# Optimization experiments

Measured on AMD Instinct MI355X. Metric: run time of the kernel, lower is better.

## Reference

```python
import jax, jax.numpy as jnp
import numpy as np

B, S, D = 2, 2048, 2048
H, DN, DR, DV, R = 16, 128, 64, 128, 512
EPS = 1e-6


def rmsnorm(x, g, eps=EPS):
    var = jnp.mean(x * x, axis=-1, keepdims=True)
    return x * jax.lax.rsqrt(var + eps) * g


def apply_rope(x, freqs):
    # x: [B,S,H,DR], freqs: [S, DR//2] angles. Complex-pair (interleaved) rotation.
    b, s, h, d = x.shape
    xp = x.reshape(b, s, h, d // 2, 2)
    xr, xi = xp[..., 0], xp[..., 1]
    cos = jnp.cos(freqs)[None, :, None, :]
    sin = jnp.sin(freqs)[None, :, None, :]
    outr = xr * cos - xi * sin
    outi = xr * sin + xi * cos
    return jnp.stack([outr, outi], axis=-1).reshape(b, s, h, d)


def setup_inputs() -> dict:
    key = jax.random.key(0)
    ks = jax.random.split(key, 8)
    x = jax.random.normal(ks[0], (B, S, D), dtype=jnp.float32)
    # RoPE angles: pos * inv_freq, standard theta=10000
    inv_freq = 1.0 / (10000.0 ** (np.arange(0, DR, 2, dtype=np.float32) / DR))
    freqs = jnp.asarray(np.arange(S, dtype=np.float32)[:, None] * inv_freq[None, :])
    sc = lambda fan_in: 1.0 / np.sqrt(fan_in)
    # weights stored [in, out] so forward is x @ W
    w_kv = jax.random.normal(ks[1], (D, R), dtype=jnp.float32) * sc(D)
    g_kv = jnp.ones((R,), dtype=jnp.float32)
    w_k = jax.random.normal(ks[2], (R, H * (DN + DR)), dtype=jnp.float32) * sc(R)
    w_v = jax.random.normal(ks[3], (R, H * DV), dtype=jnp.float32) * sc(R)
    w_qn = jax.random.normal(ks[4], (D, H * DN), dtype=jnp.float32) * sc(D)
    w_qr = jax.random.normal(ks[5], (D, H * DR), dtype=jnp.float32) * sc(D)
    w_o = jax.random.normal(ks[6], (H * DV, D), dtype=jnp.float32) * sc(H * DV)
    return {"x": x, "freqs": freqs, "w_kv": w_kv, "g_kv": g_kv, "w_k": w_k,
            "w_v": w_v, "w_qn": w_qn, "w_qr": w_qr, "w_o": w_o}


def reference(x, freqs, w_kv, g_kv, w_k, w_v, w_qn, w_qr, w_o):
    b, s, _ = x.shape
    # latent KV compression + RMSNorm
    kv = rmsnorm(x @ w_kv, g_kv)                       # [B,S,R]
    k_full = (kv @ w_k).reshape(b, s, H, DN + DR)      # [B,S,H,192]
    k_nope, k_rope = k_full[..., :DN], k_full[..., DN:]
    v = (kv @ w_v).reshape(b, s, H, DV)                # [B,S,H,DV]
    q_nope = (x @ w_qn).reshape(b, s, H, DN)
    q_rope = (x @ w_qr).reshape(b, s, H, DR)
    q_rope = apply_rope(q_rope, freqs)
    k_rope = apply_rope(k_rope, freqs)
    q = jnp.concatenate([q_nope, q_rope], axis=-1)     # [B,S,H,192]
    k = jnp.concatenate([k_nope, k_rope], axis=-1)
    scale = 1.0 / np.sqrt(DN + DR)
    scores = jnp.einsum('bshd,bthd->bhst', q, k) * scale  # [B,H,S,S]
    causal = jnp.tril(jnp.ones((s, s), dtype=bool))
    scores = jnp.where(causal[None, None], scores, jnp.float32(-1e30))
    attn = jax.nn.softmax(scores, axis=-1)
    out = jnp.einsum('bhst,bthd->bshd', attn, v).reshape(b, s, H * DV)
    return out @ w_o                                   # [B,S,D]
```

## Files before the change

### kernel.cpp

```cpp
#include <hip/hip_runtime.h>

typedef __bf16 bf16_t;
typedef bf16_t bf16x8 __attribute__((ext_vector_type(8)));
typedef bf16_t bf16x4v __attribute__((ext_vector_type(4)));
typedef float f32x4 __attribute__((ext_vector_type(4)));

#define GLDS16(g, l) __builtin_amdgcn_global_load_lds( \
    (const __attribute__((address_space(1))) void*)(g), \
    (__attribute__((address_space(3))) void*)(l), 16, 0, 0)

#define BB 2
#define SEQ 2048
#define DMODEL 2048
#define RDIM 512
#define NH 16
#define DNOPE 128
#define DROPE 64
#define DVDIM 128
#define MROWS 4096
#define DQK 192
#define KSTRIDE 3072


__global__ __launch_bounds__(256) void cast_x_kernel(const float* __restrict__ x,
                                                     bf16_t* __restrict__ xb) {
    int idx = blockIdx.x * 256 + threadIdx.x;
    float4 v = ((const float4*)x)[idx];
    bf16x4v o;
    o[0] = (bf16_t)v.x; o[1] = (bf16_t)v.y; o[2] = (bf16_t)v.z; o[3] = (bf16_t)v.w;
    ((bf16x4v*)xb)[idx] = o;
}

__global__ __launch_bounds__(256) void wtrans3_kernel(const float* __restrict__ W0,
                                                      const float* __restrict__ W1,
                                                      const float* __restrict__ W2,
                                                      int N0, int N1, int N2,
                                                      int b1, int b2,
                                                      bf16_t* __restrict__ WT, int K) {
    __shared__ float t[32][33];
    int n0 = blockIdx.x * 32, k0 = blockIdx.y * 32;
    const float* W; int Nsrc, cb;
    if (n0 < b1)      { W = W0; Nsrc = N0; cb = 0; }
    else if (n0 < b2) { W = W1; Nsrc = N1; cb = b1; }
    else              { W = W2; Nsrc = N2; cb = b2; }
    int col = n0 - cb;
    int tx = threadIdx.x & 31, ty = threadIdx.x >> 5;
    #pragma unroll
    for (int i = 0; i < 4; ++i)
        t[ty + i*8][tx] = W[(size_t)(k0 + ty + i*8) * Nsrc + col + tx];
    __syncthreads();
    #pragma unroll
    for (int i = 0; i < 4; ++i)
        WT[(size_t)(n0 + ty + i*8) * K + k0 + tx] = (bf16_t)t[tx][ty + i*8];
}

__global__ __launch_bounds__(256) void rope_table_kernel(const float* __restrict__ freqs,
                                                         float* __restrict__ costab,
                                                         float* __restrict__ sintab) {
    int idx = blockIdx.x * 256 + threadIdx.x;
    float f = freqs[idx];
    costab[idx] = cosf(f);
    sintab[idx] = sinf(f);
}

__global__ __launch_bounds__(256) void rmsnorm_kernel(const float* __restrict__ kvf,
                                                      const float* __restrict__ gkv,
                                                      bf16_t* __restrict__ kvb) {
    int m = blockIdx.x;
    int tid = threadIdx.x;
    const float* rowp = kvf + (size_t)m * RDIM;
    float2 v = *(const float2*)(rowp + tid * 2);
    float ss = v.x * v.x + v.y * v.y;
    #pragma unroll
    for (int d = 1; d < 64; d <<= 1) ss += __shfl_xor(ss, d, 64);
    __shared__ float red[4];
    if ((tid & 63) == 0) red[tid >> 6] = ss;
    __syncthreads();
    float tot = red[0] + red[1] + red[2] + red[3];
    float scale = rsqrtf(tot * (1.0f / RDIM) + 1e-6f);
    bf16_t* orow = kvb + (size_t)m * RDIM;
    orow[tid*2]     = (bf16_t)(v.x * scale * gkv[tid*2]);
    orow[tid*2 + 1] = (bf16_t)(v.y * scale * gkv[tid*2 + 1]);
}


template<typename OutT, int EPI>
__global__ __launch_bounds__(256, 3) void gemm_bt(const bf16_t* __restrict__ A,
                                                  const bf16_t* __restrict__ Bt,
                                                  OutT* __restrict__ C,
                                                  int M, int N, int K,
                                                  const float* __restrict__ costab,
                                                  const float* __restrict__ sintab,
                                                  bf16_t* __restrict__ C2) {
    __shared__ __align__(16) char ldsA[128 * 128];
    __shared__ __align__(16) char ldsB[128 * 128];
    int tid = threadIdx.x;
    int lane = tid & 63, wave = tid >> 6;
    int n0 = blockIdx.x * 128, m0 = blockIdx.y * 128;
    int wr = wave >> 1, wc = wave & 1;
    int g = lane >> 4, c = lane & 15;
    f32x4 acc[4][4] = {};

    int srow = tid >> 3;
    int sch = tid & 7;

    int nkt = K >> 6;
    for (int kt = 0; kt < nkt; ++kt) {
        int k0 = kt << 6;
        #pragma unroll
        for (int j = 0; j < 4; ++j) {
            int row = j * 32 + srow;
            int csrc = sch ^ (row & 7);
            const char* gA = (const char*)(A + (size_t)(m0 + row) * K + k0) + csrc * 16;
            const char* gB = (const char*)(Bt + (size_t)(n0 + row) * K + k0) + csrc * 16;
            char* lA = ldsA + j * 4096 + wave * 1024;
            char* lB = ldsB + j * 4096 + wave * 1024;
            GLDS16(gA, lA);
            GLDS16(gB, lB);
        }
        __syncthreads();
        #pragma unroll
        for (int kk = 0; kk < 2; ++kk) {
            int kb = kk * 64 + g * 16;
            bf16x8 aF[4], bF[4];
            #pragma unroll
            for (int m = 0; m < 4; ++m) {
                int row = wr * 64 + m * 16 + c;
                aF[m] = *(const bf16x8*)(ldsA + row * 128 + (kb ^ ((row & 7) << 4)));
            }
            #pragma unroll
            for (int n = 0; n < 4; ++n) {
                int row = wc * 64 + n * 16 + c;
                bF[n] = *(const bf16x8*)(ldsB + row * 128 + (kb ^ ((row & 7) << 4)));
            }
            #pragma unroll
            for (int m = 0; m < 4; ++m)
                #pragma unroll
                for (int n = 0; n < 4; ++n)
                    acc[m][n] = __builtin_amdgcn_mfma_f32_16x16x32_bf16(aF[m], bF[n], acc[m][n], 0, 0, 0);
        }
        __syncthreads();
    }
    #pragma unroll
    for (int m = 0; m < 4; ++m) {
        int grow0 = m0 + wr * 64 + m * 16 + g * 4;
        #pragma unroll
        for (int n = 0; n < 4; ++n) {
            int gcol = n0 + wc * 64 + n * 16 + c;
            if (EPI == 1) {
                if (gcol < 3072) {
                    bool rope = (gcol % 192) >= 128;
                    if (rope) {
                        int j = ((gcol % 192) - 128) >> 1;
                        bool even = (c & 1) == 0;
                        #pragma unroll
                        for (int i = 0; i < 4; ++i) {
                            float v = acc[m][n][i];
                            float pv = __shfl_xor(v, 1, 64);
                            int s = (grow0 + i) & (SEQ - 1);
                            float cs = costab[s * 32 + j], sn = sintab[s * 32 + j];
                            float o = even ? (v * cs - pv * sn) : (pv * sn + v * cs);
                            C[(size_t)(grow0 + i) * KSTRIDE + gcol] = (OutT)o;
                        }
                    } else {
                        #pragma unroll
                        for (int i = 0; i < 4; ++i)
                            C[(size_t)(grow0 + i) * KSTRIDE + gcol] = (OutT)acc[m][n][i];
                    }
                } else {
                    int vcol = gcol - 3072;
                    int hh = vcol >> 7, dv = vcol & 127;
                    int bb = grow0 >> 11, s = grow0 & (SEQ - 1);
                    bf16x4v o;
                    #pragma unroll
                    for (int i = 0; i < 4; ++i) o[i] = (bf16_t)acc[m][n][i];
                    *(bf16x4v*)(C2 + ((size_t)(bb * NH + hh) * 128 + dv) * SEQ + s) = o;
                }
            } else if (EPI == 3) {
                if (gcol < 512) {
                    #pragma unroll
                    for (int i = 0; i < 4; ++i)
                        C[(size_t)(grow0 + i) * 512 + gcol] = (OutT)acc[m][n][i];
                } else {
                    int qcol = gcol - 512;
                    if (qcol >= 2048) {
                        int j = ((qcol - 2048) & 63) >> 1;
                        bool even = (c & 1) == 0;
                        #pragma unroll
                        for (int i = 0; i < 4; ++i) {
                            float v = acc[m][n][i];
                            float pv = __shfl_xor(v, 1, 64);
                            int s = (grow0 + i) & (SEQ - 1);
                            float cs = costab[s * 32 + j], sn = sintab[s * 32 + j];
                            float o = even ? (v * cs - pv * sn) : (pv * sn + v * cs);
                            C2[(size_t)(grow0 + i) * 3072 + qcol] = (bf16_t)o;
                        }
                    } else {
                        #pragma unroll
                        for (int i = 0; i < 4; ++i)
                            C2[(size_t)(grow0 + i) * 3072 + qcol] = (bf16_t)acc[m][n][i];
                    }
                }
            } else {
                #pragma unroll
                for (int i = 0; i < 4; ++i)
                    C[(size_t)(grow0 + i) * N + gcol] = (OutT)acc[m][n][i];
            }
        }
    }
}


__global__ __launch_bounds__(512, 2) void attn_kernel(const bf16_t* __restrict__ Qf,
                                                      const bf16_t* __restrict__ KV,
                                                      const bf16_t* __restrict__ VT,
                                                      bf16_t* __restrict__ O) {
    __shared__ __align__(16) char ldsK[3 * 64 * 384];
    __shared__ __align__(16) char ldsV[3 * 128 * 128];
    __shared__ __align__(16) char ldsP[8 * 16 * 176];
    int tid = threadIdx.x, lane = tid & 63, wave = tid >> 6;
    int g = lane >> 4, c = lane & 15;

    int bid = blockIdx.x;
    int xcd = bid & 7, r = bid >> 3;
    int bh = xcd * 4 + (r & 3);
    int p = r >> 2;
    int b = bh >> 4, h = bh & 15;

    const bf16_t* Kb = KV + (size_t)b * SEQ * KSTRIDE + h * DQK;
    const bf16_t* Vb = VT + (size_t)bh * 128 * SEQ;
    char* ldsPw = ldsP + wave * (16 * 176);

    size_t soff[3];
    #pragma unroll
    for (int i2 = 0; i2 < 3; ++i2) {
        int id = i2 * 512 + tid;
        int row = id / 24, ch = id - row * 24;
        soff[i2] = (size_t)row * (KSTRIDE * 2) + (ch ^ (row & 7)) * 16;
    }
    size_t voff[2];
    #pragma unroll
    for (int i2 = 0; i2 < 2; ++i2) {
        int id = i2 * 512 + tid;
        int row = id >> 3, ch = id & 7;
        voff[i2] = (size_t)row * (SEQ * 2) + (ch ^ (row & 7)) * 16;
    }
    const float sc = 0.0721687836f * 1.44269504f;

    bf16x8 vones;
    #pragma unroll
    for (int j = 0; j < 8; ++j) vones[j] = (bf16_t)1.0f;

    auto stage = [&](int t, int buf) {
        const char* Kt = (const char*)Kb + (size_t)t * (64 * KSTRIDE * 2);
        #pragma unroll
        for (int i2 = 0; i2 < 3; ++i2)
            GLDS16(Kt + soff[i2], ldsK + buf * 24576 + i2 * 8192 + wave * 1024);
        const char* Vt = (const char*)Vb + (size_t)t * 128;
        #pragma unroll
        for (int i2 = 0; i2 < 2; ++i2)
            GLDS16(Vt + voff[i2], ldsV + buf * 16384 + i2 * 8192 + wave * 1024);
    };

    #pragma unroll 1
    for (int pass = 0; pass < 2; ++pass) {
        int qt = pass ? p : (15 - p);
        int q0 = qt * 128;
        int nt = 2 * qt + 2;
        int tdiag = 2 * qt + (wave >> 2);

        bf16x8 qf[6];
        {
            int qrow = q0 + wave * 16 + c;
            const bf16_t* qn = Qf + (size_t)(b * SEQ + qrow) * 3072 + h * DNOPE + g * 8;
            #pragma unroll
            for (int kk = 0; kk < 4; ++kk) qf[kk] = *(const bf16x8*)(qn + kk * 32);
            const bf16_t* qr = Qf + (size_t)(b * SEQ + qrow) * 3072 + 2048 + h * DROPE + g * 8;
            qf[4] = *(const bf16x8*)(qr);
            qf[5] = *(const bf16x8*)(qr + 32);
            #pragma unroll
            for (int kk = 0; kk < 6; ++kk)
                #pragma unroll
                for (int j = 0; j < 8; ++j)
                    qf[kk][j] = (bf16_t)((float)qf[kk][j] * sc);
        }
        float m_run[4];
        f32x4 accO[9] = {};
        #pragma unroll
        for (int i = 0; i < 4; ++i) m_run[i] = -3.0e38f;

        stage(0, 0);
        stage(1, 1);

        #pragma unroll 1
        for (int t = 0; t < nt; ++t) {
            int cur = t - (t / 3) * 3;
            if (t + 1 < nt) asm volatile("s_waitcnt vmcnt(5)" ::: "memory");
            else            asm volatile("s_waitcnt vmcnt(0)" ::: "memory");
            __builtin_amdgcn_s_barrier();
            __builtin_amdgcn_sched_barrier(0);
            asm volatile("" ::: "memory");
            if (t + 2 < nt) stage(t + 2, (t + 2) % 3);

            if (t <= tdiag) {
                bool diag = (t == tdiag);
                const char* ldsKc = ldsK + cur * 24576;
                const char* ldsVc = ldsV + cur * 16384;

                f32x4 accS[4] = {};
                __builtin_amdgcn_s_setprio(1);
                #pragma unroll
                for (int kk = 0; kk < 6; ++kk) {
                    int kb = kk * 64 + g * 16;
                    #pragma unroll
                    for (int n = 0; n < 4; ++n) {
                        int row = n * 16 + c;
                        bf16x8 kf = *(const bf16x8*)(ldsKc + row * 384 + (kb ^ ((row & 7) << 4)));
                        accS[n] = __builtin_amdgcn_mfma_f32_16x16x32_bf16(qf[kk], kf, accS[n], 0, 0, 0);
                    }
                }
                __builtin_amdgcn_s_setprio(0);

                if (diag) {
                    #pragma unroll
                    for (int n = 0; n < 4; ++n)
                        #pragma unroll
                        for (int i = 0; i < 4; ++i)
                            if (n * 16 + c > (wave & 3) * 16 + g * 4 + i) accS[n][i] = -1e30f;
                }
                float mloc[4];
                #pragma unroll
                for (int i = 0; i < 4; ++i)
                    mloc[i] = fmaxf(fmaxf(accS[0][i], accS[1][i]), fmaxf(accS[2][i], accS[3][i]));
                bool cheap = __all((mloc[0] <= m_run[0] + 8.f) & (mloc[1] <= m_run[1] + 8.f) &
                                   (mloc[2] <= m_run[2] + 8.f) & (mloc[3] <= m_run[3] + 8.f));
                if (cheap) {
                    #pragma unroll
                    for (int i = 0; i < 4; ++i)
                        #pragma unroll
                        for (int n = 0; n < 4; ++n)
                            accS[n][i] = exp2f(accS[n][i] - m_run[i]);
                } else {
                    #pragma unroll
                    for (int i = 0; i < 4; ++i) {
                        float m2 = mloc[i];
                        #pragma unroll
                        for (int d = 1; d < 16; d <<= 1) m2 = fmaxf(m2, __shfl_xor(m2, d, 64));
                        float mnew = fmaxf(m_run[i], m2);
                        float alpha = exp2f(m_run[i] - mnew);
                        m_run[i] = mnew;
                        #pragma unroll
                        for (int n = 0; n < 4; ++n)
                            accS[n][i] = exp2f(accS[n][i] - mnew);
                        #pragma unroll
                        for (int n = 0; n < 9; ++n) accO[n][i] *= alpha;
                    }
                }
                #pragma unroll
                for (int n = 0; n < 4; ++n)
                    #pragma unroll
                    for (int i = 0; i < 4; ++i)
                        *(bf16_t*)(ldsPw + (g * 4 + i) * 176 + (n * 16 + c) * 2) = (bf16_t)accS[n][i];
                bf16x8 pf0 = *(const bf16x8*)(ldsPw + c * 176 + g * 16);
                bf16x8 pf1 = *(const bf16x8*)(ldsPw + c * 176 + 64 + g * 16);

                __builtin_amdgcn_s_setprio(1);
                #pragma unroll
                for (int n = 0; n < 8; ++n) {
                    int row = n * 16 + c;
                    bf16x8 vf0 = *(const bf16x8*)(ldsVc + row * 128 + ((g * 16) ^ ((c & 7) << 4)));
                    bf16x8 vf1 = *(const bf16x8*)(ldsVc + row * 128 + ((64 + g * 16) ^ ((c & 7) << 4)));
                    accO[n] = __builtin_amdgcn_mfma_f32_16x16x32_bf16(pf0, vf0, accO[n], 0, 0, 0);
                    accO[n] = __builtin_amdgcn_mfma_f32_16x16x32_bf16(pf1, vf1, accO[n], 0, 0, 0);
                }
                accO[8] = __builtin_amdgcn_mfma_f32_16x16x32_bf16(pf0, vones, accO[8], 0, 0, 0);
                accO[8] = __builtin_amdgcn_mfma_f32_16x16x32_bf16(pf1, vones, accO[8], 0, 0, 0);
                __builtin_amdgcn_s_setprio(0);
            }
        }
        float inv_l[4];
        #pragma unroll
        for (int i = 0; i < 4; ++i) inv_l[i] = 1.0f / accO[8][i];
        #pragma unroll
        for (int n = 0; n < 8; ++n) {
            int gcol = h * 128 + n * 16 + c;
            #pragma unroll
            for (int i = 0; i < 4; ++i) {
                int mrow = b * SEQ + q0 + wave * 16 + g * 4 + i;
                O[(size_t)mrow * 2048 + gcol] = (bf16_t)(accO[n][i] * inv_l[i]);
            }
        }
        __syncthreads();
    }
}


extern "C" void kernel_launch(void* const* d_in, const int* in_sizes, int n_in,
                              void* d_out, int out_size, void* d_ws, size_t ws_size,
                              hipStream_t stream) {
    const float* x     = (const float*)d_in[0];
    const float* freqs = (const float*)d_in[1];
    const float* w_kv  = (const float*)d_in[2];
    const float* g_kv  = (const float*)d_in[3];
    const float* w_k   = (const float*)d_in[4];
    const float* w_v   = (const float*)d_in[5];
    const float* w_qn  = (const float*)d_in[6];
    const float* w_qr  = (const float*)d_in[7];
    const float* w_o   = (const float*)d_in[8];
    float* out = (float*)d_out;

    char* ws = (char*)d_ws;
    size_t off = 0;
    auto alloc = [&](size_t bytes) { char* p = ws + off; off += (bytes + 255) & ~(size_t)255; return p; };
    bf16_t* xb     = (bf16_t*)alloc((size_t)MROWS * DMODEL * 2);
    bf16_t* wqkT   = (bf16_t*)alloc((size_t)3584 * DMODEL * 2);
    bf16_t* wkvwT  = (bf16_t*)alloc((size_t)5120 * RDIM * 2);
    bf16_t* woT    = (bf16_t*)alloc((size_t)DMODEL * DMODEL * 2);
    float*  kvf    = (float*) alloc((size_t)MROWS * RDIM * 4);
    bf16_t* kvb    = (bf16_t*)alloc((size_t)MROWS * RDIM * 2);
    bf16_t* kvout  = (bf16_t*)alloc((size_t)MROWS * KSTRIDE * 2);
    bf16_t* qfull  = (bf16_t*)alloc((size_t)MROWS * 3072 * 2);
    bf16_t* vt     = (bf16_t*)alloc((size_t)32 * 128 * SEQ * 2);
    bf16_t* attno  = (bf16_t*)alloc((size_t)MROWS * 2048 * 2);
    float*  costab = (float*) alloc((size_t)SEQ * 32 * 4);
    float*  sintab = (float*) alloc((size_t)SEQ * 32 * 4);

    cast_x_kernel<<<(MROWS * DMODEL / 4) / 256, 256, 0, stream>>>(x, xb);
    wtrans3_kernel<<<dim3(3584 / 32, DMODEL / 32), 256, 0, stream>>>(
        w_kv, w_qn, w_qr, 512, 2048, 1024, 512, 2560, wqkT, DMODEL);
    wtrans3_kernel<<<dim3(5120 / 32, RDIM / 32), 256, 0, stream>>>(
        w_k, w_v, w_v, 3072, 2048, 2048, 3072, 5120, wkvwT, RDIM);
    wtrans3_kernel<<<dim3(2048 / 32, DMODEL / 32), 256, 0, stream>>>(
        w_o, w_o, w_o, 2048, 2048, 2048, 2048, 4096, woT, DMODEL);
    rope_table_kernel<<<(SEQ * 32) / 256, 256, 0, stream>>>(freqs, costab, sintab);

    gemm_bt<float, 3><<<dim3(3584 / 128, MROWS / 128), 256, 0, stream>>>(
        xb, wqkT, kvf, MROWS, 3584, DMODEL, costab, sintab, qfull);
    rmsnorm_kernel<<<MROWS, 256, 0, stream>>>(kvf, g_kv, kvb);
    gemm_bt<bf16_t, 1><<<dim3(5120 / 128, MROWS / 128), 256, 0, stream>>>(
        kvb, wkvwT, kvout, MROWS, 5120, RDIM, costab, sintab, vt);

    attn_kernel<<<256, 512, 0, stream>>>(qfull, kvout, vt, attno);

    gemm_bt<float, 0><<<dim3(2048 / 128, MROWS / 128), 256, 0, stream>>>(
        attno, woT, out, MROWS, 2048, DMODEL, nullptr, nullptr, nullptr);
}
```

Before: 277.3 us.

## Split attention into one q-tile per block, load V directly from global

Each attention block now processes a single 128-row query tile rather than two paired passes, and the grid doubles to 512 blocks. V tiles are no longer staged through LDS; each wave reads V fragments straight from global memory into registers before the PV MFMAs. K staging drops from triple to double buffering with a full vmcnt(0) wait each iteration. This cuts LDS use and should raise occupancy, but it adds uncoalesced global V reads that are repeated across waves, shortens the prefetch distance, and gives up the balanced causal pairing, so blocks now carry uneven work.

```diff
diff --git a/kernel.cpp b/kernel.cpp
--- a/kernel.cpp
+++ b/kernel.cpp
@@ -215,17 +215,20 @@
                                                       const bf16_t* __restrict__ KV,
                                                       const bf16_t* __restrict__ VT,
                                                       bf16_t* __restrict__ O) {
-    __shared__ __align__(16) char ldsK[3 * 64 * 384];
-    __shared__ __align__(16) char ldsV[3 * 128 * 128];
+    __shared__ __align__(16) char ldsK[2 * 64 * 384];
     __shared__ __align__(16) char ldsP[8 * 16 * 176];
     int tid = threadIdx.x, lane = tid & 63, wave = tid >> 6;
     int g = lane >> 4, c = lane & 15;
 
     int bid = blockIdx.x;
-    int xcd = bid & 7, r = bid >> 3;
-    int bh = xcd * 4 + (r & 3);
-    int p = r >> 2;
+    int xcd = bid & 7, rest = bid >> 3;
+    int bh = xcd * 4 + (rest & 3);
+    int slot = rest >> 2;
+    int qt = (slot < 8) ? (15 - slot) : (slot - 8);
     int b = bh >> 4, h = bh & 15;
+    int q0 = qt * 128;
+    int nt = 2 * qt + 2;
+    int tdiag = 2 * qt + (wave >> 2);
 
     const bf16_t* Kb = KV + (size_t)b * SEQ * KSTRIDE + h * DQK;
     const bf16_t* Vb = VT + (size_t)bh * 128 * SEQ;
@@ -238,13 +241,6 @@
         int row = id / 24, ch = id - row * 24;
         soff[i2] = (size_t)row * (KSTRIDE * 2) + (ch ^ (row & 7)) * 16;
     }
-    size_t voff[2];
-    #pragma unroll
-    for (int i2 = 0; i2 < 2; ++i2) {
-        int id = i2 * 512 + tid;
-        int row = id >> 3, ch = id & 7;
-        voff[i2] = (size_t)row * (SEQ * 2) + (ch ^ (row & 7)) * 16;
-    }
     const float sc = 0.0721687836f * 1.44269504f;
 
     bf16x8 vones;
@@ -256,141 +252,141 @@
         #pragma unroll
         for (int i2 = 0; i2 < 3; ++i2)
             GLDS16(Kt + soff[i2], ldsK + buf * 24576 + i2 * 8192 + wave * 1024);
-        const char* Vt = (const char*)Vb + (size_t)t * 128;
-        #pragma unroll
-        for (int i2 = 0; i2 < 2; ++i2)
-            GLDS16(Vt + voff[i2], ldsV + buf * 16384 + i2 * 8192 + wave * 1024);
     };
 
+    bf16x8 qf[6];
+    {
+        int qrow = q0 + wave * 16 + c;
+        const bf16_t* qn = Qf + (size_t)(b * SEQ + qrow) * 3072 + h * DNOPE + g * 8;
+        #pragma unroll
+        for (int kk = 0; kk < 4; ++kk) qf[kk] = *(const bf16x8*)(qn + kk * 32);
+        const bf16_t* qr = Qf + (size_t)(b * SEQ + qrow) * 3072 + 2048 + h * DROPE + g * 8;
+        qf[4] = *(const bf16x8*)(qr);
+        qf[5] = *(const bf16x8*)(qr + 32);
+        #pragma unroll
+        for (int kk = 0; kk < 6; ++kk)
+            #pragma unroll
+            for (int j = 0; j < 8; ++j)
+                qf[kk][j] = (bf16_t)((float)qf[kk][j] * sc);
+    }
+    float m_run[4];
+    f32x4 accO[9] = {};
+    #pragma unroll
+    for (int i = 0; i < 4; ++i) m_run[i] = -3.0e38f;
+
+    stage(0, 0);
+
     #pragma unroll 1
-    for (int pass = 0; pass < 2; ++pass) {
-        int qt = pass ? p : (15 - p);
-        int q0 = qt * 128;
-        int nt = 2 * qt + 2;
-        int tdiag = 2 * qt + (wave >> 2);
-
-        bf16x8 qf[6];
-        {
-            int qrow = q0 + wave * 16 + c;
-            const bf16_t* qn = Qf + (size_t)(b * SEQ + qrow) * 3072 + h * DNOPE + g * 8;
-            #pragma unroll
-            for (int kk = 0; kk < 4; ++kk) qf[kk] = *(const bf16x8*)(qn + kk * 32);
-            const bf16_t* qr = Qf + (size_t)(b * SEQ + qrow) * 3072 + 2048 + h * DROPE + g * 8;
-            qf[4] = *(const bf16x8*)(qr);
-            qf[5] = *(const bf16x8*)(qr + 32);
-            #pragma unroll
-            for (int kk = 0; kk < 6; ++kk)
-                #pragma unroll
-                for (int j = 0; j < 8; ++j)
-                    qf[kk][j] = (bf16_t)((float)qf[kk][j] * sc);
+    for (int t = 0; t < nt; ++t) {
+        int cur = t & 1;
+        asm volatile("s_waitcnt vmcnt(0)" ::: "memory");
+        __builtin_amdgcn_s_barrier();
+        __builtin_amdgcn_sched_barrier(0);
+        if (t + 1 < nt) stage(t + 1, cur ^ 1);
+
+        if (t <= tdiag) {
+            bool diag = (t == tdiag);
+            const char* ldsKc = ldsK + cur * 24576;
+
+            f32x4 accS[4] = {};
+            __builtin_amdgcn_s_setprio(1);
+            #pragma unroll
+            for (int kk = 0; kk < 6; ++kk) {
+                int kb = kk * 64 + g * 16;
+                #pragma unroll
+                for (int n = 0; n < 4; ++n) {
+                    int row = n * 16 + c;
+                    bf16x8 kf = *(const bf16x8*)(ldsKc + row * 384 + (kb ^ ((row & 7) << 4)));
+                    accS[n] = __builtin_amdgcn_mfma_f32_16x16x32_bf16(qf[kk], kf, accS[n], 0, 0, 0);
+                }
+            }
+            __builtin_amdgcn_s_setprio(0);
+
+            if (diag) {
+                #pragma unroll
+                for (int n = 0; n < 4; ++n)
+                    #pragma unroll
+                    for (int i = 0; i < 4; ++i)
+                        if (n * 16 + c > (wave & 3) * 16 + g * 4 + i) accS[n][i] = -1e30f;
+            }
+            float mloc[4];
+            #pragma unroll
+            for (int i = 0; i < 4; ++i)
+                mloc[i] = fmaxf(fmaxf(accS[0][i], accS[1][i]), fmaxf(accS[2][i], accS[3][i]));
+            bool cheap = __all((mloc[0] <= m_run[0] + 8.f) & (mloc[1] <= m_run[1] + 8.f) &
+                               (mloc[2] <= m_run[2] + 8.f) & (mloc[3] <= m_run[3] + 8.f));
+            if (cheap) {
+                #pragma unroll
+                for (int i = 0; i < 4; ++i)
+                    #pragma unroll
+                    for (int n = 0; n < 4; ++n)
+                        accS[n][i] = exp2f(accS[n][i] - m_run[i]);
+            } else {
+                #pragma unroll
+                for (int i = 0; i < 4; ++i) {
+                    float m2 = mloc[i];
+                    #pragma unroll
+                    for (int d = 1; d < 16; d <<= 1) m2 = fmaxf(m2, __shfl_xor(m2, d, 64));
+                    float mnew = fmaxf(m_run[i], m2);
+                    float alpha = exp2f(m_run[i] - mnew);
+                    m_run[i] = mnew;
+                    #pragma unroll
+                    for (int n = 0; n < 4; ++n)
+                        accS[n][i] = exp2f(accS[n][i] - mnew);
+                    #pragma unroll
+                    for (int n = 0; n < 9; ++n) accO[n][i] *= alpha;
+                }
+            }
+            #pragma unroll
+            for (int n = 0; n < 4; ++n)
+                #pragma unroll
+                for (int i = 0; i < 4; ++i)
+                    *(bf16_t*)(ldsPw + (g * 4 + i) * 176 + (n * 16 + c) * 2) = (bf16_t)accS[n][i];
+            bf16x8 pf0 = *(const bf16x8*)(ldsPw + c * 176 + g * 16);
+            bf16x8 pf1 = *(const bf16x8*)(ldsPw + c * 176 + 64 + g * 16);
+
+            __builtin_amdgcn_s_setprio(1);
+            {
+                bf16x8 vf[8];
+                #pragma unroll
+                for (int n = 0; n < 4; ++n) {
+                    const bf16_t* vrow = Vb + (size_t)(n * 16 + c) * SEQ + t * 64 + g * 8;
+                    vf[2 * n]     = *(const bf16x8*)(vrow);
+                    vf[2 * n + 1] = *(const bf16x8*)(vrow + 32);
+                }
+                #pragma unroll
+                for (int n = 0; n < 4; ++n) {
+                    accO[n] = __builtin_amdgcn_mfma_f32_16x16x32_bf16(pf0, vf[2 * n],     accO[n], 0, 0, 0);
+                    accO[n] = __builtin_amdgcn_mfma_f32_16x16x32_bf16(pf1, vf[2 * n + 1], accO[n], 0, 0, 0);
+                }
+                #pragma unroll
+                for (int n = 0; n < 4; ++n) {
+                    const bf16_t* vrow = Vb + (size_t)((n + 4) * 16 + c) * SEQ + t * 64 + g * 8;
+                    vf[2 * n]     = *(const bf16x8*)(vrow);
+                    vf[2 * n + 1] = *(const bf16x8*)(vrow + 32);
+                }
+                #pragma unroll
+                for (int n = 0; n < 4; ++n) {
+                    accO[n + 4] = __builtin_amdgcn_mfma_f32_16x16x32_bf16(pf0, vf[2 * n],     accO[n + 4], 0, 0, 0);
+                    accO[n + 4] = __builtin_amdgcn_mfma_f32_16x16x32_bf16(pf1, vf[2 * n + 1], accO[n + 4], 0, 0, 0);
+                }
+            }
+            accO[8] = __builtin_amdgcn_mfma_f32_16x16x32_bf16(pf0, vones, accO[8], 0, 0, 0);
+            accO[8] = __builtin_amdgcn_mfma_f32_16x16x32_bf16(pf1, vones, accO[8], 0, 0, 0);
+            __builtin_amdgcn_s_setprio(0);
         }
-        float m_run[4];
-        f32x4 accO[9] = {};
-        #pragma unroll
-        for (int i = 0; i < 4; ++i) m_run[i] = -3.0e38f;
-
-        stage(0, 0);
-        stage(1, 1);
-
-        #pragma unroll 1
-        for (int t = 0; t < nt; ++t) {
-            int cur = t - (t / 3) * 3;
-            if (t + 1 < nt) asm volatile("s_waitcnt vmcnt(5)" ::: "memory");
-            else            asm volatile("s_waitcnt vmcnt(0)" ::: "memory");
-            __builtin_amdgcn_s_barrier();
-            __builtin_amdgcn_sched_barrier(0);
-            asm volatile("" ::: "memory");
-            if (t + 2 < nt) stage(t + 2, (t + 2) % 3);
-
-            if (t <= tdiag) {
-                bool diag = (t == tdiag);
-                const char* ldsKc = ldsK + cur * 24576;
-                const char* ldsVc = ldsV + cur * 16384;
-
-                f32x4 accS[4] = {};
-                __builtin_amdgcn_s_setprio(1);
-                #pragma unroll
-                for (int kk = 0; kk < 6; ++kk) {
-                    int kb = kk * 64 + g * 16;
-                    #pragma unroll
-                    for (int n = 0; n < 4; ++n) {
-                        int row = n * 16 + c;
-                        bf16x8 kf = *(const bf16x8*)(ldsKc + row * 384 + (kb ^ ((row & 7) << 4)));
-                        accS[n] = __builtin_amdgcn_mfma_f32_16x16x32_bf16(qf[kk], kf, accS[n], 0, 0, 0);
-                    }
-                }
-                __builtin_amdgcn_s_setprio(0);
-
-                if (diag) {
-                    #pragma unroll
-                    for (int n = 0; n < 4; ++n)
-                        #pragma unroll
-                        for (int i = 0; i < 4; ++i)
-                            if (n * 16 + c > (wave & 3) * 16 + g * 4 + i) accS[n][i] = -1e30f;
-                }
-                float mloc[4];
-                #pragma unroll
-                for (int i = 0; i < 4; ++i)
-                    mloc[i] = fmaxf(fmaxf(accS[0][i], accS[1][i]), fmaxf(accS[2][i], accS[3][i]));
-                bool cheap = __all((mloc[0] <= m_run[0] + 8.f) & (mloc[1] <= m_run[1] + 8.f) &
-                                   (mloc[2] <= m_run[2] + 8.f) & (mloc[3] <= m_run[3] + 8.f));
-                if (cheap) {
-                    #pragma unroll
-                    for (int i = 0; i < 4; ++i)
-                        #pragma unroll
-                        for (int n = 0; n < 4; ++n)
-                            accS[n][i] = exp2f(accS[n][i] - m_run[i]);
-                } else {
-                    #pragma unroll
-                    for (int i = 0; i < 4; ++i) {
-                        float m2 = mloc[i];
-                        #pragma unroll
-                        for (int d = 1; d < 16; d <<= 1) m2 = fmaxf(m2, __shfl_xor(m2, d, 64));
-                        float mnew = fmaxf(m_run[i], m2);
-                        float alpha = exp2f(m_run[i] - mnew);
-                        m_run[i] = mnew;
-                        #pragma unroll
-                        for (int n = 0; n < 4; ++n)
-                            accS[n][i] = exp2f(accS[n][i] - mnew);
-                        #pragma unroll
-                        for (int n = 0; n < 9; ++n) accO[n][i] *= alpha;
-                    }
-                }
-                #pragma unroll
-                for (int n = 0; n < 4; ++n)
-                    #pragma unroll
-                    for (int i = 0; i < 4; ++i)
-                        *(bf16_t*)(ldsPw + (g * 4 + i) * 176 + (n * 16 + c) * 2) = (bf16_t)accS[n][i];
-                bf16x8 pf0 = *(const bf16x8*)(ldsPw + c * 176 + g * 16);
-                bf16x8 pf1 = *(const bf16x8*)(ldsPw + c * 176 + 64 + g * 16);
-
-                __builtin_amdgcn_s_setprio(1);
-                #pragma unroll
-                for (int n = 0; n < 8; ++n) {
-                    int row = n * 16 + c;
-                    bf16x8 vf0 = *(const bf16x8*)(ldsVc + row * 128 + ((g * 16) ^ ((c & 7) << 4)));
-                    bf16x8 vf1 = *(const bf16x8*)(ldsVc + row * 128 + ((64 + g * 16) ^ ((c & 7) << 4)));
-                    accO[n] = __builtin_amdgcn_mfma_f32_16x16x32_bf16(pf0, vf0, accO[n], 0, 0, 0);
-                    accO[n] = __builtin_amdgcn_mfma_f32_16x16x32_bf16(pf1, vf1, accO[n], 0, 0, 0);
-                }
-                accO[8] = __builtin_amdgcn_mfma_f32_16x16x32_bf16(pf0, vones, accO[8], 0, 0, 0);
-                accO[8] = __builtin_amdgcn_mfma_f32_16x16x32_bf16(pf1, vones, accO[8], 0, 0, 0);
-                __builtin_amdgcn_s_setprio(0);
-            }
+    }
+    float inv_l[4];
+    #pragma unroll
+    for (int i = 0; i < 4; ++i) inv_l[i] = 1.0f / accO[8][i];
+    #pragma unroll
+    for (int n = 0; n < 8; ++n) {
+        int gcol = h * 128 + n * 16 + c;
+        #pragma unroll
+        for (int i = 0; i < 4; ++i) {
+            int mrow = b * SEQ + q0 + wave * 16 + g * 4 + i;
+            O[(size_t)mrow * 2048 + gcol] = (bf16_t)(accO[n][i] * inv_l[i]);
         }
-        float inv_l[4];
-        #pragma unroll
-        for (int i = 0; i < 4; ++i) inv_l[i] = 1.0f / accO[8][i];
-        #pragma unroll
-        for (int n = 0; n < 8; ++n) {
-            int gcol = h * 128 + n * 16 + c;
-            #pragma unroll
-            for (int i = 0; i < 4; ++i) {
-                int mrow = b * SEQ + q0 + wave * 16 + g * 4 + i;
-                O[(size_t)mrow * 2048 + gcol] = (bf16_t)(accO[n][i] * inv_l[i]);
-            }
-        }
-        __syncthreads();
     }
 }
 
@@ -440,7 +436,7 @@
     gemm_bt<bf16_t, 1><<<dim3(5120 / 128, MROWS / 128), 256, 0, stream>>>(
         kvb, wkvwT, kvout, MROWS, 5120, RDIM, costab, sintab, vt);
 
-    attn_kernel<<<256, 512, 0, stream>>>(qfull, kvout, vt, attno);
+    attn_kernel<<<512, 512, 0, stream>>>(qfull, kvout, vt, attno);
 
     gemm_bt<float, 0><<<dim3(2048 / 128, MROWS / 128), 256, 0, stream>>>(
         attno, woT, out, MROWS, 2048, DMODEL, nullptr, nullptr, nullptr);
```

New measurement: 418.5 us. 50.9% more time.

## Triple-buffer GEMM LDS pipeline with 512-thread 128x256 tiles

Applied to the files above, without the earlier changes.

Rewrites the shared bf16 GEMM to use 8 waves per block with a 128x256 output tile. Global-to-LDS loads now run two k-tiles ahead through a three-stage LDS ring, synchronised with explicit vmcnt waits and a single barrier per iteration. MFMA sections are raised in priority with s_setprio. The intent is to hide global load latency and halve B-tile reloads. In exchange, LDS use rises to about 144KB and occupancy drops to one block per CU, and the grids become smaller, for example 14x32 for the first GEMM.

```diff
diff --git a/kernel.cpp b/kernel.cpp
--- a/kernel.cpp
+++ b/kernel.cpp
@@ -85,53 +85,70 @@
 
 
 template<typename OutT, int EPI>
-__global__ __launch_bounds__(256, 3) void gemm_bt(const bf16_t* __restrict__ A,
+__global__ __launch_bounds__(512, 1) void gemm_bt(const bf16_t* __restrict__ A,
                                                   const bf16_t* __restrict__ Bt,
                                                   OutT* __restrict__ C,
                                                   int M, int N, int K,
                                                   const float* __restrict__ costab,
                                                   const float* __restrict__ sintab,
                                                   bf16_t* __restrict__ C2) {
-    __shared__ __align__(16) char ldsA[128 * 128];
-    __shared__ __align__(16) char ldsB[128 * 128];
+    __shared__ __align__(16) char ldsA[3 * 128 * 128];
+    __shared__ __align__(16) char ldsB[3 * 256 * 128];
     int tid = threadIdx.x;
     int lane = tid & 63, wave = tid >> 6;
-    int n0 = blockIdx.x * 128, m0 = blockIdx.y * 128;
-    int wr = wave >> 1, wc = wave & 1;
+    int wm = wave >> 2, wn = wave & 3;
+    int n0 = blockIdx.x * 256, m0 = blockIdx.y * 128;
     int g = lane >> 4, c = lane & 15;
     f32x4 acc[4][4] = {};
 
-    int srow = tid >> 3;
-    int sch = tid & 7;
+    auto stage = [&](int t, int buf) {
+        int k0 = t << 6;
+        #pragma unroll
+        for (int i = 0; i < 2; ++i) {
+            int id = i * 512 + tid;
+            int row = id >> 3, ch = id & 7;
+            GLDS16((const char*)(A + (size_t)(m0 + row) * K + k0) + ((ch ^ (row & 7)) * 16),
+                   ldsA + buf * 16384 + i * 8192 + wave * 1024);
+        }
+        #pragma unroll
+        for (int i = 0; i < 4; ++i) {
+            int id = i * 512 + tid;
+            int row = id >> 3, ch = id & 7;
+            GLDS16((const char*)(Bt + (size_t)(n0 + row) * K + k0) + ((ch ^ (row & 7)) * 16),
+                   ldsB + buf * 32768 + i * 8192 + wave * 1024);
+        }
+    };
 
     int nkt = K >> 6;
-    for (int kt = 0; kt < nkt; ++kt) {
-        int k0 = kt << 6;
-        #pragma unroll
-        for (int j = 0; j < 4; ++j) {
-            int row = j * 32 + srow;
-            int csrc = sch ^ (row & 7);
-            const char* gA = (const char*)(A + (size_t)(m0 + row) * K + k0) + csrc * 16;
-            const char* gB = (const char*)(Bt + (size_t)(n0 + row) * K + k0) + csrc * 16;
-            char* lA = ldsA + j * 4096 + wave * 1024;
-            char* lB = ldsB + j * 4096 + wave * 1024;
-            GLDS16(gA, lA);
-            GLDS16(gB, lB);
-        }
-        __syncthreads();
+    stage(0, 0);
+    stage(1, 1);
+
+    #pragma unroll 1
+    for (int t = 0; t < nkt; ++t) {
+        int buf = t - (t / 3) * 3;
+        if (t + 1 < nkt) asm volatile("s_waitcnt vmcnt(6)" ::: "memory");
+        else             asm volatile("s_waitcnt vmcnt(0)" ::: "memory");
+        __builtin_amdgcn_s_barrier();
+        __builtin_amdgcn_sched_barrier(0);
+        asm volatile("" ::: "memory");
+        if (t + 2 < nkt) stage(t + 2, (t + 2) % 3);
+
+        const char* lA = ldsA + buf * 16384;
+        const char* lB = ldsB + buf * 32768;
+        __builtin_amdgcn_s_setprio(1);
         #pragma unroll
         for (int kk = 0; kk < 2; ++kk) {
             int kb = kk * 64 + g * 16;
             bf16x8 aF[4], bF[4];
             #pragma unroll
             for (int m = 0; m < 4; ++m) {
-                int row = wr * 64 + m * 16 + c;
-                aF[m] = *(const bf16x8*)(ldsA + row * 128 + (kb ^ ((row & 7) << 4)));
+                int row = wm * 64 + m * 16 + c;
+                aF[m] = *(const bf16x8*)(lA + row * 128 + (kb ^ ((row & 7) << 4)));
             }
             #pragma unroll
             for (int n = 0; n < 4; ++n) {
-                int row = wc * 64 + n * 16 + c;
-                bF[n] = *(const bf16x8*)(ldsB + row * 128 + (kb ^ ((row & 7) << 4)));
+                int row = wn * 64 + n * 16 + c;
+                bF[n] = *(const bf16x8*)(lB + row * 128 + (kb ^ ((row & 7) << 4)));
             }
             #pragma unroll
             for (int m = 0; m < 4; ++m)
@@ -139,14 +156,14 @@
                 for (int n = 0; n < 4; ++n)
                     acc[m][n] = __builtin_amdgcn_mfma_f32_16x16x32_bf16(aF[m], bF[n], acc[m][n], 0, 0, 0);
         }
-        __syncthreads();
+        __builtin_amdgcn_s_setprio(0);
     }
     #pragma unroll
     for (int m = 0; m < 4; ++m) {
-        int grow0 = m0 + wr * 64 + m * 16 + g * 4;
+        int grow0 = m0 + wm * 64 + m * 16 + g * 4;
         #pragma unroll
         for (int n = 0; n < 4; ++n) {
-            int gcol = n0 + wc * 64 + n * 16 + c;
+            int gcol = n0 + wn * 64 + n * 16 + c;
             if (EPI == 1) {
                 if (gcol < 3072) {
                     bool rope = (gcol % 192) >= 128;
@@ -434,14 +451,14 @@
         w_o, w_o, w_o, 2048, 2048, 2048, 2048, 4096, woT, DMODEL);
     rope_table_kernel<<<(SEQ * 32) / 256, 256, 0, stream>>>(freqs, costab, sintab);
 
-    gemm_bt<float, 3><<<dim3(3584 / 128, MROWS / 128), 256, 0, stream>>>(
+    gemm_bt<float, 3><<<dim3(3584 / 256, MROWS / 128), 512, 0, stream>>>(
         xb, wqkT, kvf, MROWS, 3584, DMODEL, costab, sintab, qfull);
     rmsnorm_kernel<<<MROWS, 256, 0, stream>>>(kvf, g_kv, kvb);
-    gemm_bt<bf16_t, 1><<<dim3(5120 / 128, MROWS / 128), 256, 0, stream>>>(
+    gemm_bt<bf16_t, 1><<<dim3(5120 / 256, MROWS / 128), 512, 0, stream>>>(
         kvb, wkvwT, kvout, MROWS, 5120, RDIM, costab, sintab, vt);
 
     attn_kernel<<<256, 512, 0, stream>>>(qfull, kvout, vt, attno);
 
-    gemm_bt<float, 0><<<dim3(2048 / 128, MROWS / 128), 256, 0, stream>>>(
+    gemm_bt<float, 0><<<dim3(2048 / 256, MROWS / 128), 512, 0, stream>>>(
         attno, woT, out, MROWS, 2048, DMODEL, nullptr, nullptr, nullptr);
 }
```

Result: slower. 317.6 us (+14.6%).

## Process 32 query rows per wave in attention with 4-wave blocks

Applied to the files above, without the earlier changes.

The attention kernel now uses 256 threads (4 waves) per block instead of 512, and each wave handles two 16-row query groups. Every K and V fragment read from LDS is reused for two MFMAs, halving LDS traffic per unit of compute. Staging loops issue twice as many global-to-LDS loads per thread, and the vmcnt wait is adjusted to match. The cost is roughly double the accumulator registers per wave and fewer waves per block to hide latency, with occupancy hinted at one block per SIMD set.

```diff
diff --git a/kernel.cpp b/kernel.cpp
--- a/kernel.cpp
+++ b/kernel.cpp
@@ -211,13 +211,13 @@
 }
 
 
-__global__ __launch_bounds__(512, 2) void attn_kernel(const bf16_t* __restrict__ Qf,
+__global__ __launch_bounds__(256, 1) void attn_kernel(const bf16_t* __restrict__ Qf,
                                                       const bf16_t* __restrict__ KV,
                                                       const bf16_t* __restrict__ VT,
                                                       bf16_t* __restrict__ O) {
     __shared__ __align__(16) char ldsK[3 * 64 * 384];
     __shared__ __align__(16) char ldsV[3 * 128 * 128];
-    __shared__ __align__(16) char ldsP[8 * 16 * 176];
+    __shared__ __align__(16) char ldsP[4 * 32 * 176];
     int tid = threadIdx.x, lane = tid & 63, wave = tid >> 6;
     int g = lane >> 4, c = lane & 15;
 
@@ -229,19 +229,19 @@
 
     const bf16_t* Kb = KV + (size_t)b * SEQ * KSTRIDE + h * DQK;
     const bf16_t* Vb = VT + (size_t)bh * 128 * SEQ;
-    char* ldsPw = ldsP + wave * (16 * 176);
-
-    size_t soff[3];
-    #pragma unroll
-    for (int i2 = 0; i2 < 3; ++i2) {
-        int id = i2 * 512 + tid;
+    char* ldsPw = ldsP + wave * (32 * 176);
+
+    size_t soff[6];
+    #pragma unroll
+    for (int i2 = 0; i2 < 6; ++i2) {
+        int id = i2 * 256 + tid;
         int row = id / 24, ch = id - row * 24;
         soff[i2] = (size_t)row * (KSTRIDE * 2) + (ch ^ (row & 7)) * 16;
     }
-    size_t voff[2];
-    #pragma unroll
-    for (int i2 = 0; i2 < 2; ++i2) {
-        int id = i2 * 512 + tid;
+    size_t voff[4];
+    #pragma unroll
+    for (int i2 = 0; i2 < 4; ++i2) {
+        int id = i2 * 256 + tid;
         int row = id >> 3, ch = id & 7;
         voff[i2] = (size_t)row * (SEQ * 2) + (ch ^ (row & 7)) * 16;
     }
@@ -254,12 +254,12 @@
     auto stage = [&](int t, int buf) {
         const char* Kt = (const char*)Kb + (size_t)t * (64 * KSTRIDE * 2);
         #pragma unroll
-        for (int i2 = 0; i2 < 3; ++i2)
-            GLDS16(Kt + soff[i2], ldsK + buf * 24576 + i2 * 8192 + wave * 1024);
+        for (int i2 = 0; i2 < 6; ++i2)
+            GLDS16(Kt + soff[i2], ldsK + buf * 24576 + i2 * 4096 + wave * 1024);
         const char* Vt = (const char*)Vb + (size_t)t * 128;
         #pragma unroll
-        for (int i2 = 0; i2 < 2; ++i2)
-            GLDS16(Vt + voff[i2], ldsV + buf * 16384 + i2 * 8192 + wave * 1024);
+        for (int i2 = 0; i2 < 4; ++i2)
+            GLDS16(Vt + voff[i2], ldsV + buf * 16384 + i2 * 4096 + wave * 1024);
     };
 
     #pragma unroll 1
@@ -267,15 +267,17 @@
         int qt = pass ? p : (15 - p);
         int q0 = qt * 128;
         int nt = 2 * qt + 2;
-        int tdiag = 2 * qt + (wave >> 2);
-
-        bf16x8 qf[6];
-        {
-            int qrow = q0 + wave * 16 + c;
+        int tdiag = 2 * qt + (wave >> 1);
+
+        bf16x8 qf0[6], qf1[6];
+        #pragma unroll
+        for (int grp = 0; grp < 2; ++grp) {
+            int qrow = q0 + wave * 32 + grp * 16 + c;
             const bf16_t* qn = Qf + (size_t)(b * SEQ + qrow) * 3072 + h * DNOPE + g * 8;
+            const bf16_t* qr = Qf + (size_t)(b * SEQ + qrow) * 3072 + 2048 + h * DROPE + g * 8;
+            bf16x8* qf = grp ? qf1 : qf0;
             #pragma unroll
             for (int kk = 0; kk < 4; ++kk) qf[kk] = *(const bf16x8*)(qn + kk * 32);
-            const bf16_t* qr = Qf + (size_t)(b * SEQ + qrow) * 3072 + 2048 + h * DROPE + g * 8;
             qf[4] = *(const bf16x8*)(qr);
             qf[5] = *(const bf16x8*)(qr + 32);
             #pragma unroll
@@ -284,10 +286,12 @@
                 for (int j = 0; j < 8; ++j)
                     qf[kk][j] = (bf16_t)((float)qf[kk][j] * sc);
         }
-        float m_run[4];
-        f32x4 accO[9] = {};
-        #pragma unroll
-        for (int i = 0; i < 4; ++i) m_run[i] = -3.0e38f;
+        float m_run[2][4];
+        f32x4 accO[2][9] = {};
+        #pragma unroll
+        for (int grp = 0; grp < 2; ++grp)
+            #pragma unroll
+            for (int i = 0; i < 4; ++i) m_run[grp][i] = -3.0e38f;
 
         stage(0, 0);
         stage(1, 1);
@@ -295,7 +299,7 @@
         #pragma unroll 1
         for (int t = 0; t < nt; ++t) {
             int cur = t - (t / 3) * 3;
-            if (t + 1 < nt) asm volatile("s_waitcnt vmcnt(5)" ::: "memory");
+            if (t + 1 < nt) asm volatile("s_waitcnt vmcnt(10)" ::: "memory");
             else            asm volatile("s_waitcnt vmcnt(0)" ::: "memory");
             __builtin_amdgcn_s_barrier();
             __builtin_amdgcn_sched_barrier(0);
@@ -307,7 +311,7 @@
                 const char* ldsKc = ldsK + cur * 24576;
                 const char* ldsVc = ldsV + cur * 16384;
 
-                f32x4 accS[4] = {};
+                f32x4 accS0[4] = {}, accS1[4] = {};
                 __builtin_amdgcn_s_setprio(1);
                 #pragma unroll
                 for (int kk = 0; kk < 6; ++kk) {
@@ -316,53 +320,77 @@
                     for (int n = 0; n < 4; ++n) {
                         int row = n * 16 + c;
                         bf16x8 kf = *(const bf16x8*)(ldsKc + row * 384 + (kb ^ ((row & 7) << 4)));
-                        accS[n] = __builtin_amdgcn_mfma_f32_16x16x32_bf16(qf[kk], kf, accS[n], 0, 0, 0);
+                        accS0[n] = __builtin_amdgcn_mfma_f32_16x16x32_bf16(qf0[kk], kf, accS0[n], 0, 0, 0);
+                        accS1[n] = __builtin_amdgcn_mfma_f32_16x16x32_bf16(qf1[kk], kf, accS1[n], 0, 0, 0);
                     }
                 }
                 __builtin_amdgcn_s_setprio(0);
 
                 if (diag) {
+                    int rbase = (wave & 1) * 32 + g * 4;
                     #pragma unroll
                     for (int n = 0; n < 4; ++n)
                         #pragma unroll
-                        for (int i = 0; i < 4; ++i)
-                            if (n * 16 + c > (wave & 3) * 16 + g * 4 + i) accS[n][i] = -1e30f;
-                }
-                float mloc[4];
-                #pragma unroll
-                for (int i = 0; i < 4; ++i)
-                    mloc[i] = fmaxf(fmaxf(accS[0][i], accS[1][i]), fmaxf(accS[2][i], accS[3][i]));
-                bool cheap = __all((mloc[0] <= m_run[0] + 8.f) & (mloc[1] <= m_run[1] + 8.f) &
-                                   (mloc[2] <= m_run[2] + 8.f) & (mloc[3] <= m_run[3] + 8.f));
+                        for (int i = 0; i < 4; ++i) {
+                            if (n * 16 + c > rbase + i)      accS0[n][i] = -1e30f;
+                            if (n * 16 + c > rbase + 16 + i) accS1[n][i] = -1e30f;
+                        }
+                }
+                float ml0[4], ml1[4];
+                #pragma unroll
+                for (int i = 0; i < 4; ++i) {
+                    ml0[i] = fmaxf(fmaxf(accS0[0][i], accS0[1][i]), fmaxf(accS0[2][i], accS0[3][i]));
+                    ml1[i] = fmaxf(fmaxf(accS1[0][i], accS1[1][i]), fmaxf(accS1[2][i], accS1[3][i]));
+                }
+                bool cheap = __all((ml0[0] <= m_run[0][0] + 8.f) & (ml0[1] <= m_run[0][1] + 8.f) &
+                                   (ml0[2] <= m_run[0][2] + 8.f) & (ml0[3] <= m_run[0][3] + 8.f) &
+                                   (ml1[0] <= m_run[1][0] + 8.f) & (ml1[1] <= m_run[1][1] + 8.f) &
+                                   (ml1[2] <= m_run[1][2] + 8.f) & (ml1[3] <= m_run[1][3] + 8.f));
                 if (cheap) {
                     #pragma unroll
                     for (int i = 0; i < 4; ++i)
                         #pragma unroll
-                        for (int n = 0; n < 4; ++n)
-                            accS[n][i] = exp2f(accS[n][i] - m_run[i]);
+                        for (int n = 0; n < 4; ++n) {
+                            accS0[n][i] = exp2f(accS0[n][i] - m_run[0][i]);
+                            accS1[n][i] = exp2f(accS1[n][i] - m_run[1][i]);
+                        }
                 } else {
                     #pragma unroll
                     for (int i = 0; i < 4; ++i) {
-                        float m2 = mloc[i];
-                        #pragma unroll
-                        for (int d = 1; d < 16; d <<= 1) m2 = fmaxf(m2, __shfl_xor(m2, d, 64));
-                        float mnew = fmaxf(m_run[i], m2);
-                        float alpha = exp2f(m_run[i] - mnew);
-                        m_run[i] = mnew;
-                        #pragma unroll
-                        for (int n = 0; n < 4; ++n)
-                            accS[n][i] = exp2f(accS[n][i] - mnew);
-                        #pragma unroll
-                        for (int n = 0; n < 9; ++n) accO[n][i] *= alpha;
+                        float m20 = ml0[i], m21 = ml1[i];
+                        #pragma unroll
+                        for (int d = 1; d < 16; d <<= 1) {
+                            m20 = fmaxf(m20, __shfl_xor(m20, d, 64));
+                            m21 = fmaxf(m21, __shfl_xor(m21, d, 64));
+                        }
+                        float mn0 = fmaxf(m_run[0][i], m20);
+                        float mn1 = fmaxf(m_run[1][i], m21);
+                        float a0 = exp2f(m_run[0][i] - mn0);
+                        float a1 = exp2f(m_run[1][i] - mn1);
+                        m_run[0][i] = mn0; m_run[1][i] = mn1;
+                        #pragma unroll
+                        for (int n = 0; n < 4; ++n) {
+                            accS0[n][i] = exp2f(accS0[n][i] - mn0);
+                            accS1[n][i] = exp2f(accS1[n][i] - mn1);
+                        }
+                        #pragma unroll
+                        for (int n = 0; n < 9; ++n) {
+                            accO[0][n][i] *= a0;
+                            accO[1][n][i] *= a1;
+                        }
                     }
                 }
                 #pragma unroll
                 for (int n = 0; n < 4; ++n)
                     #pragma unroll
-                    for (int i = 0; i < 4; ++i)
-                        *(bf16_t*)(ldsPw + (g * 4 + i) * 176 + (n * 16 + c) * 2) = (bf16_t)accS[n][i];
-                bf16x8 pf0 = *(const bf16x8*)(ldsPw + c * 176 + g * 16);
-                bf16x8 pf1 = *(const bf16x8*)(ldsPw + c * 176 + 64 + g * 16);
+                    for (int i = 0; i < 4; ++i) {
+                        *(bf16_t*)(ldsPw + (g * 4 + i) * 176 + (n * 16 + c) * 2)        = (bf16_t)accS0[n][i];
+                        *(bf16_t*)(ldsPw + (16 + g * 4 + i) * 176 + (n * 16 + c) * 2)   = (bf16_t)accS1[n][i];
+                    }
+                bf16x8 pf00 = *(const bf16x8*)(ldsPw + c * 176 + g * 16);
+                bf16x8 pf01 = *(const bf16x8*)(ldsPw + c * 176 + 64 + g * 16);
+                bf16x8 pf10 = *(const bf16x8*)(ldsPw + (16 + c) * 176 + g * 16);
+                bf16x8 pf11 = *(const bf16x8*)(ldsPw + (16 + c) * 176 + 64 + g * 16);
 
                 __builtin_amdgcn_s_setprio(1);
                 #pragma unroll
@@ -370,24 +398,31 @@
                     int row = n * 16 + c;
                     bf16x8 vf0 = *(const bf16x8*)(ldsVc + row * 128 + ((g * 16) ^ ((c & 7) << 4)));
                     bf16x8 vf1 = *(const bf16x8*)(ldsVc + row * 128 + ((64 + g * 16) ^ ((c & 7) << 4)));
-                    accO[n] = __builtin_amdgcn_mfma_f32_16x16x32_bf16(pf0, vf0, accO[n], 0, 0, 0);
-                    accO[n] = __builtin_amdgcn_mfma_f32_16x16x32_bf16(pf1, vf1, accO[n], 0, 0, 0);
-                }
-                accO[8] = __builtin_amdgcn_mfma_f32_16x16x32_bf16(pf0, vones, accO[8], 0, 0, 0);
-                accO[8] = __builtin_amdgcn_mfma_f32_16x16x32_bf16(pf1, vones, accO[8], 0, 0, 0);
+                    accO[0][n] = __builtin_amdgcn_mfma_f32_16x16x32_bf16(pf00, vf0, accO[0][n], 0, 0, 0);
+                    accO[0][n] = __builtin_amdgcn_mfma_f32_16x16x32_bf16(pf01, vf1, accO[0][n], 0, 0, 0);
+                    accO[1][n] = __builtin_amdgcn_mfma_f32_16x16x32_bf16(pf10, vf0, accO[1][n], 0, 0, 0);
+                    accO[1][n] = __builtin_amdgcn_mfma_f32_16x16x32_bf16(pf11, vf1, accO[1][n], 0, 0, 0);
+                }
+                accO[0][8] = __builtin_amdgcn_mfma_f32_16x16x32_bf16(pf00, vones, accO[0][8], 0, 0, 0);
+                accO[0][8] = __builtin_amdgcn_mfma_f32_16x16x32_bf16(pf01, vones, accO[0][8], 0, 0, 0);
+                accO[1][8] = __builtin_amdgcn_mfma_f32_16x16x32_bf16(pf10, vones, accO[1][8], 0, 0, 0);
+                accO[1][8] = __builtin_amdgcn_mfma_f32_16x16x32_bf16(pf11, vones, accO[1][8], 0, 0, 0);
                 __builtin_amdgcn_s_setprio(0);
             }
         }
-        float inv_l[4];
-        #pragma unroll
-        for (int i = 0; i < 4; ++i) inv_l[i] = 1.0f / accO[8][i];
-        #pragma unroll
-        for (int n = 0; n < 8; ++n) {
-            int gcol = h * 128 + n * 16 + c;
-            #pragma unroll
-            for (int i = 0; i < 4; ++i) {
-                int mrow = b * SEQ + q0 + wave * 16 + g * 4 + i;
-                O[(size_t)mrow * 2048 + gcol] = (bf16_t)(accO[n][i] * inv_l[i]);
+        #pragma unroll
+        for (int grp = 0; grp < 2; ++grp) {
+            float inv_l[4];
+            #pragma unroll
+            for (int i = 0; i < 4; ++i) inv_l[i] = 1.0f / accO[grp][8][i];
+            #pragma unroll
+            for (int n = 0; n < 8; ++n) {
+                int gcol = h * 128 + n * 16 + c;
+                #pragma unroll
+                for (int i = 0; i < 4; ++i) {
+                    int mrow = b * SEQ + q0 + wave * 32 + grp * 16 + g * 4 + i;
+                    O[(size_t)mrow * 2048 + gcol] = (bf16_t)(accO[grp][n][i] * inv_l[i]);
+                }
             }
         }
         __syncthreads();
@@ -440,7 +475,7 @@
     gemm_bt<bf16_t, 1><<<dim3(5120 / 128, MROWS / 128), 256, 0, stream>>>(
         kvb, wkvwT, kvout, MROWS, 5120, RDIM, costab, sintab, vt);
 
-    attn_kernel<<<256, 512, 0, stream>>>(qfull, kvout, vt, attno);
+    attn_kernel<<<256, 256, 0, stream>>>(qfull, kvout, vt, attno);
 
     gemm_bt<float, 0><<<dim3(2048 / 128, MROWS / 128), 256, 0, stream>>>(
         attno, woT, out, MROWS, 2048, DMODEL, nullptr, nullptr, nullptr);
```

Measured after the change: 304.7 us. +9.9%, slower.
